# Kernel optimization log

Hardware: AMD Instinct MI355X
Metric: run time of the kernel (lower is better)

The kernel has to match this reference:

```python
import jax, jax.numpy as jnp
import numpy as np

B, N, NC = 16, 128, 32          # batch, num_vectors, num_condition_vectors
H, A, DEG = 256, 64, 3          # hidden_dim, attention_dim, degree
SCALE = float(np.sqrt(H) ** DEG)  # weights_scale = sqrt(hidden_dim)^degree = 4096
# S3 non-identity permutations lifted to batch tensor axes (batch axis 0 fixed)
PERMS = [(0, 1, 3, 2), (0, 2, 1, 3), (0, 2, 3, 1), (0, 3, 1, 2), (0, 3, 2, 1)]


def setup_inputs() -> dict:
    key = jax.random.key(0)
    ks = jax.random.split(key, 6)
    inv = 1.0 / np.sqrt(H)
    return {
        "x": jax.random.normal(ks[0], (B, N, H), jnp.float32),
        "x_mask": jnp.ones((B, N, 1), jnp.float32),
        "condition": jax.random.normal(ks[1], (B, NC, H), jnp.float32),
        "condition_mask": jnp.ones((B, NC, 1), jnp.float32),
        "W1": (jax.random.normal(ks[2], (DEG, H, H), jnp.float32) * inv),
        "b1": jnp.zeros((DEG, H), jnp.float32),
        "Wc": (jax.random.normal(ks[3], (DEG, H, H), jnp.float32) * inv),
        "Wlin": (jax.random.normal(ks[4], (DEG, H, A), jnp.float32) * inv),
        "blin": jnp.zeros((DEG, A), jnp.float32),
    }


def reference(x, x_mask, condition, condition_mask, W1, b1, Wc, Wlin, blin):
    # masked mean-pool of condition vectors: [B, H]
    pooled = (condition * condition_mask).sum(1) / jnp.maximum(condition_mask.sum(1), 1.0)
    ys, dvs = [], []
    for d in range(DEG):  # small fixed loop over structurally distinct branches
        dv = pooled @ Wc[d]                                   # daughter vector [B, H]
        h = jax.nn.gelu(x @ W1[d] + b1[d] + dv[:, None, :])   # branch encoder [B, N, H]
        y = (h @ Wlin[d] + blin[d]) * x_mask                  # linear + mask  [B, N, A]
        ys.append(y)
        dvs.append(dv)
    # degree-3 multilinear contraction: 'xbi,ybi,zbi->bxyz' == 'bxi,byi,bzi->bxyz'
    base = jnp.einsum('bxi,byi,bzi->bxyz', ys[0], ys[1], ys[2]) / SCALE
    # symmetrize: add all non-identity permuted views (S3 minus identity)
    out = base
    for p in PERMS:
        out = out + jnp.transpose(base, p)
    return out, jnp.stack(dvs)  # ([B,N,N,N], [DEG,B,H])
```

## Files before the change

### kernel.cpp

```cpp
#include <hip/hip_runtime.h>
#include <hip/hip_bf16.h>
#include <math.h>
#include <string.h>

#define BB   16
#define NN   128
#define NCC  32
#define HH   256
#define AA   64
#define DEGN 3
#define BNR  (BB*NN)

typedef __bf16 bf16x8 __attribute__((ext_vector_type(8)));
typedef float  f32x16 __attribute__((ext_vector_type(16)));

__device__ __forceinline__ unsigned int pk2(float lo, float hi) {
    __hip_bfloat162 h2 = __float22bfloat162_rn(make_float2(lo, hi));
    unsigned int u;
    memcpy(&u, &h2, 4);
    return u;
}
__device__ __forceinline__ float2 unpk(unsigned int u) {
    return make_float2(__uint_as_float(u << 16),
                       __uint_as_float(u & 0xffff0000u));
}
__device__ __forceinline__ unsigned short bfbits(float f) {
    __hip_bfloat16 h = __float2bfloat16(f);
    unsigned short u;
    memcpy(&u, &h, 2);
    return u;
}

__global__ __launch_bounds__(256) void k_head(const float* __restrict__ cond,
                                              const float* __restrict__ cmask,
                                              const float* __restrict__ Wc,
                                              const float* __restrict__ W1,
                                              const float* __restrict__ Wlin,
                                              float* __restrict__ dv,
                                              float* __restrict__ dv_out,
                                              unsigned short* __restrict__ W1t,
                                              unsigned short* __restrict__ Wlt) {
    __shared__ float shm[32 * 33];
    const int bid = blockIdx.x, t = threadIdx.x;

    if (bid < 48) {
        const int d = bid >> 4, b = bid & 15;
        float s = 0.f, ms = 0.f;
        for (int c = 0; c < NCC; ++c) {
            float mk = cmask[b * NCC + c];
            s  += cond[(b * NCC + c) * HH + t] * mk;
            ms += mk;
        }
        shm[t] = s / fmaxf(ms, 1.0f);
        __syncthreads();
        const float* Wd = Wc + (size_t)d * HH * HH;
        float acc = 0.f;
        for (int k = 0; k < HH; ++k) acc += shm[k] * Wd[k * HH + t];
        int idx = (d * BB + b) * HH + t;
        dv[idx]     = acc;
        dv_out[idx] = acc;
    } else if (bid < 240) {
        const int q = bid - 48;
        const int d = q >> 6, r2 = q & 63, tk = r2 >> 3, tn = r2 & 7;
        float (*tile)[33] = (float (*)[33])shm;
        #pragma unroll
        for (int p = 0; p < 4; ++p) {
            int kr = p * 8 + (t >> 5), nr = t & 31;
            tile[kr][nr] = W1[((size_t)d * HH + tk * 32 + kr) * HH + tn * 32 + nr];
        }
        __syncthreads();
        #pragma unroll
        for (int p = 0; p < 4; ++p) {
            int nr = p * 8 + (t >> 5), kr = t & 31;
            W1t[((size_t)d * HH + tn * 32 + nr) * HH + tk * 32 + kr] =
                bfbits(tile[kr][nr]);
        }
    } else {
        const int q = bid - 240;
        const int d = q >> 4, r3 = q & 15, tk = r3 >> 1, ta = r3 & 1;
        float (*tile)[33] = (float (*)[33])shm;
        #pragma unroll
        for (int p = 0; p < 4; ++p) {
            int kr = p * 8 + (t >> 5), ar = t & 31;
            tile[kr][ar] = Wlin[((size_t)d * HH + tk * 32 + kr) * AA + ta * 32 + ar];
        }
        __syncthreads();
        #pragma unroll
        for (int p = 0; p < 4; ++p) {
            int ar = p * 8 + (t >> 5), kr = t & 31;
            Wlt[((size_t)d * AA + ta * 32 + ar) * HH + tk * 32 + kr] =
                bfbits(tile[kr][ar]);
        }
    }
}

__global__ __launch_bounds__(256) void k_mlp(const float* __restrict__ x,
                                             const float* __restrict__ xmask,
                                             const float* __restrict__ b1,
                                             const float* __restrict__ blin,
                                             const float* __restrict__ dv,
                                             const unsigned short* __restrict__ W1t,
                                             const unsigned short* __restrict__ Wlt,
                                             float* __restrict__ yv) {
    __shared__ __align__(16) char ldsA[32 * 512];
    __shared__ float ps[2][32][68];

    const int t = threadIdx.x;
    const int d = blockIdx.x >> 6, rt = blockIdx.x & 63;
    const int row0 = rt * 32;
    const int b = row0 >> 7;
    const int lane = t & 63, wid = t >> 6;
    const int rl5 = lane & 31, h2v = lane >> 5;

    #pragma unroll
    for (int it = 0; it < 8; ++it) {
        const int r = wid * 8 + it;
        const float4 v = *(const float4*)&x[(size_t)(row0 + r) * HH + lane * 4];
        uint2 u = make_uint2(pk2(v.x, v.y), pk2(v.z, v.w));
        *(uint2*)(ldsA + r * 512 + ((lane * 8) ^ ((r & 7) << 4))) = u;
    }
    __syncthreads();

    f32x16 acc1[2];
    #pragma unroll
    for (int nt = 0; nt < 2; ++nt)
        #pragma unroll
        for (int e = 0; e < 16; ++e) acc1[nt][e] = 0.f;

    #pragma unroll
    for (int ks = 0; ks < 16; ++ks) {
        bf16x8 af = *(const bf16x8*)(ldsA + rl5 * 512 +
                      ((ks * 32 + h2v * 16) ^ ((rl5 & 7) << 4)));
        #pragma unroll
        for (int nt = 0; nt < 2; ++nt) {
            const int n = wid * 64 + nt * 32 + rl5;
            bf16x8 bf = *(const bf16x8*)(W1t +
                          ((size_t)d * HH + n) * HH + ks * 16 + h2v * 8);
            acc1[nt] = __builtin_amdgcn_mfma_f32_32x32x16_bf16(af, bf, acc1[nt], 0, 0, 0);
        }
    }
    __syncthreads();

    #pragma unroll
    for (int nt = 0; nt < 2; ++nt) {
        const int col = wid * 64 + nt * 32 + rl5;
        const float add = b1[d * HH + col] + dv[(d * BB + b) * HH + col];
        #pragma unroll
        for (int e = 0; e < 16; ++e) {
            const int row = (e & 3) + 8 * (e >> 2) + 4 * h2v;
            float v = acc1[nt][e] + add;
            float u = 0.7978845608028654f * (v + 0.044715f * v * v * v);
            float g = 0.5f * v * (1.0f + tanhf(u));
            *(unsigned short*)(ldsA + row * 512 + ((col * 2) ^ ((row & 7) << 4))) =
                bfbits(g);
        }
    }
    __syncthreads();

    const int qc = wid >> 1, kh = wid & 1;
    f32x16 acc2;
    #pragma unroll
    for (int e = 0; e < 16; ++e) acc2[e] = 0.f;
    #pragma unroll
    for (int ks = 0; ks < 8; ++ks) {
        const int kk = kh * 8 + ks;
        bf16x8 af = *(const bf16x8*)(ldsA + rl5 * 512 +
                      ((kk * 32 + h2v * 16) ^ ((rl5 & 7) << 4)));
        bf16x8 bf = *(const bf16x8*)(Wlt +
                      ((size_t)d * AA + qc * 32 + rl5) * HH + kk * 16 + h2v * 8);
        acc2 = __builtin_amdgcn_mfma_f32_32x32x16_bf16(af, bf, acc2, 0, 0, 0);
    }
    #pragma unroll
    for (int e = 0; e < 16; ++e) {
        const int row = (e & 3) + 8 * (e >> 2) + 4 * h2v;
        ps[kh][row][qc * 32 + rl5] = acc2[e];
    }
    __syncthreads();

    #pragma unroll
    for (int j = 0; j < 8; ++j) {
        const int idx = t * 8 + j;
        const int row = idx >> 6, a = idx & 63;
        float v = ps[0][row][a] + ps[1][row][a] + blin[d * AA + a];
        v *= xmask[row0 + row];
        yv[((size_t)d * BNR + row0 + row) * AA + a] = v;
    }
}

__device__ __forceinline__ void lds_fence_barrier() {
    asm volatile("s_waitcnt lgkmcnt(0)" ::: "memory");
    __builtin_amdgcn_s_barrier();
    __builtin_amdgcn_sched_barrier(0);
}
__device__ __forceinline__ void lds_wave_wait() {
    asm volatile("s_waitcnt lgkmcnt(0)" ::: "memory");
    __builtin_amdgcn_sched_barrier(0);
}

#define LROW 128

__global__ __launch_bounds__(512, 4) void k_contract(const float* __restrict__ yv,
                                                     float* __restrict__ outp) {
    __shared__ __align__(16) char lds[5 * 128 * LROW];
    char* A1b = lds;
    char* A2b = lds + 1 * 128 * LROW;
    char* Y0b = lds + 2 * 128 * LROW;
    char* B1b = lds + 3 * 128 * LROW;
    char* B2b = lds + 4 * 128 * LROW;

    const int t  = threadIdx.x;
    const int b  = blockIdx.x >> 5;
    const int xg = blockIdx.x & 31;

    const float* y0p = yv + (size_t)(0 * BNR + b * NN) * AA;
    const float* y1p = yv + (size_t)(1 * BNR + b * NN) * AA;
    const float* y2p = yv + (size_t)(2 * BNR + b * NN) * AA;

    const int lane = t & 63;
    const int wid  = t >> 6;
    const int li   = lane & 31;
    const int rh   = lane >> 5;
    const int rl5  = lane & 31, h2v = lane >> 5;
    const int wr   = wid >> 1, wc = wid & 1;

    float s0v[4], s1v[4], s2v[4];
    #pragma unroll
    for (int xi = 0; xi < 4; ++xi) {
        const int xr = xg * 4 + xi;
        s0v[xi] = y0p[xr * AA + lane];
        s1v[xi] = y1p[xr * AA + lane];
        s2v[xi] = y2p[xr * AA + lane];
    }

    #pragma unroll
    for (int it = 0; it < 8; ++it) {
        const int r   = wid * 16 + it * 2 + rh;
        const int swz = (r & 7) << 4;
        const int off = r * LROW + ((4 * li) ^ swz);
        const float2 v0 = *(const float2*)&y0p[r * AA + 2 * li];
        const float2 v1 = *(const float2*)&y1p[r * AA + 2 * li];
        const float2 v2 = *(const float2*)&y2p[r * AA + 2 * li];
        *(unsigned int*)(Y0b + off) = pk2(v0.x, v0.y);
        *(unsigned int*)(B1b + off) = pk2(v2.x, v2.y);
        *(unsigned int*)(B2b + off) = pk2(v1.x, v1.y);
    }

    const float inv = 1.0f / 4096.0f;
    float* scrf = (float*)(A1b + wid * 2048);

    #pragma unroll
    for (int xi = 0; xi < 4; ++xi) {
        const int xr = xg * 4 + xi;
        const float s0a = __shfl(s0v[xi], 2 * li), s0b = __shfl(s0v[xi], 2 * li + 1);
        const float s1a = __shfl(s1v[xi], 2 * li), s1b = __shfl(s1v[xi], 2 * li + 1);
        const float s2a = __shfl(s2v[xi], 2 * li), s2b = __shfl(s2v[xi], 2 * li + 1);

        if (xi == 0) lds_fence_barrier();

        #pragma unroll
        for (int it = 0; it < 8; ++it) {
            const int r   = wid * 16 + it * 2 + rh;
            const int swz = (r & 7) << 4;
            const int off = r * LROW + ((4 * li) ^ swz);
            const float2 y0 = unpk(*(const unsigned int*)(Y0b + off));
            const float2 y1 = unpk(*(const unsigned int*)(B2b + off));
            *(unsigned int*)(A1b + off) =
                pk2(s0a * y1.x + s1a * y0.x, s0b * y1.y + s1b * y0.y);
            *(unsigned int*)(A2b + off) = pk2(s2a * y0.x, s2b * y0.y);
        }
        lds_fence_barrier();

        f32x16 acc[2];
        #pragma unroll
        for (int ni = 0; ni < 2; ++ni)
            #pragma unroll
            for (int e = 0; e < 16; ++e) acc[ni][e] = 0.f;

        #pragma unroll
        for (int p = 0; p < 4; ++p) {
            const char* Ua = (p == 0) ? A1b : (p == 1) ? B1b : (p == 2) ? A2b : B2b;
            const char* Va = (p == 0) ? B1b : (p == 1) ? A1b : (p == 2) ? B2b : A2b;
            #pragma unroll
            for (int ks = 0; ks < 4; ++ks) {
                const int arow = wr * 32 + rl5;
                bf16x8 af = *(const bf16x8*)(Ua + arow * LROW +
                              ((ks * 32 + h2v * 16) ^ ((arow & 7) << 4)));
                #pragma unroll
                for (int ni = 0; ni < 2; ++ni) {
                    const int brow = wc * 64 + ni * 32 + rl5;
                    bf16x8 bf = *(const bf16x8*)(Va + brow * LROW +
                                  ((ks * 32 + h2v * 16) ^ ((brow & 7) << 4)));
                    acc[ni] = __builtin_amdgcn_mfma_f32_32x32x16_bf16(
                        af, bf, acc[ni], 0, 0, 0);
                }
            }
        }
        lds_fence_barrier();

        float* osl = outp + ((size_t)(b * NN + xr)) * (NN * NN);
        #pragma unroll
        for (int q = 0; q < 4; ++q) {
            #pragma unroll
            for (int ni = 0; ni < 2; ++ni) {
                #pragma unroll
                for (int j = 0; j < 4; ++j) {
                    const int e = q * 4 + j;
                    scrf[(j + 4 * h2v) * 64 + ni * 32 + rl5] = acc[ni][e] * inv;
                }
            }
            lds_wave_wait();
            #pragma unroll
            for (int r2 = 0; r2 < 8; ++r2) {
                float v = scrf[r2 * 64 + lane];
                osl[(size_t)(wr * 32 + q * 8 + r2) * NN + wc * 64 + lane] = v;
            }
            lds_wave_wait();
        }
    }
}

extern "C" void kernel_launch(void* const* d_in, const int* in_sizes, int n_in,
                              void* d_out, int out_size, void* d_ws, size_t ws_size,
                              hipStream_t stream) {
    const float* x     = (const float*)d_in[0];
    const float* xmask = (const float*)d_in[1];
    const float* cond  = (const float*)d_in[2];
    const float* cmask = (const float*)d_in[3];
    const float* W1    = (const float*)d_in[4];
    const float* b1    = (const float*)d_in[5];
    const float* Wc    = (const float*)d_in[6];
    const float* Wlin  = (const float*)d_in[7];
    const float* blin  = (const float*)d_in[8];

    float* out = (float*)d_out;
    float* ws  = (float*)d_ws;

    float* dv  = ws;
    float* yv  = ws + 12288;
    unsigned short* W1t = (unsigned short*)((char*)d_ws + (size_t)(12288 + 393216) * 4);
    unsigned short* Wlt = W1t + (size_t)DEGN * HH * HH;
    float* dv_out = out + (size_t)BB * NN * NN * NN;

    k_head    <<<dim3(288), dim3(256), 0, stream>>>(cond, cmask, Wc, W1, Wlin,
                                                    dv, dv_out, W1t, Wlt);
    k_mlp     <<<dim3(DEGN * 64), dim3(256), 0, stream>>>(x, xmask, b1, blin, dv,
                                                          W1t, Wlt, yv);
    k_contract<<<dim3(BB * NN / 4), dim3(512), 0, stream>>>(yv, out);
}
```

Before: 58.88 us.

## Overlap output stores with next slice MFMAs and drop LDS staging

The contraction kernel now double-buffers its accumulators, so the global stores for slice xi-1 are interleaved with the MFMA loop of slice xi instead of running after it. B rows are remapped to interleave the two 32-column tiles (brow = 2*rl5+ni), which lets each lane write adjacent float2 pairs directly to global memory and removes the LDS scratch transpose. The swizzle is changed to depend on r>>1 to match the new row access pattern. This costs extra accumulator registers and relies on float2 stores being coalesced well enough.

```diff
diff --git a/kernel.cpp b/kernel.cpp
--- a/kernel.cpp
+++ b/kernel.cpp
@@ -192,12 +192,9 @@
     __builtin_amdgcn_s_barrier();
     __builtin_amdgcn_sched_barrier(0);
 }
-__device__ __forceinline__ void lds_wave_wait() {
-    asm volatile("s_waitcnt lgkmcnt(0)" ::: "memory");
-    __builtin_amdgcn_sched_barrier(0);
-}
 
 #define LROW 128
+#define SWZ(r) ((((r) >> 1) & 7) << 4)
 
 __global__ __launch_bounds__(512, 4) void k_contract(const float* __restrict__ yv,
                                                      float* __restrict__ outp) {
@@ -222,6 +219,7 @@
     const int rh   = lane >> 5;
     const int rl5  = lane & 31, h2v = lane >> 5;
     const int wr   = wid >> 1, wc = wid & 1;
+    const float inv = 1.0f / 4096.0f;
 
     float s0v[4], s1v[4], s2v[4];
     #pragma unroll
@@ -235,8 +233,7 @@
     #pragma unroll
     for (int it = 0; it < 8; ++it) {
         const int r   = wid * 16 + it * 2 + rh;
-        const int swz = (r & 7) << 4;
-        const int off = r * LROW + ((4 * li) ^ swz);
+        const int off = r * LROW + ((4 * li) ^ SWZ(r));
         const float2 v0 = *(const float2*)&y0p[r * AA + 2 * li];
         const float2 v1 = *(const float2*)&y1p[r * AA + 2 * li];
         const float2 v2 = *(const float2*)&y2p[r * AA + 2 * li];
@@ -245,23 +242,18 @@
         *(unsigned int*)(B2b + off) = pk2(v1.x, v1.y);
     }
 
-    const float inv = 1.0f / 4096.0f;
-    float* scrf = (float*)(A1b + wid * 2048);
-
-    #pragma unroll
-    for (int xi = 0; xi < 4; ++xi) {
-        const int xr = xg * 4 + xi;
+    f32x16 accA[2], accB[2];
+
+    auto xi_step = [&](int xi, f32x16 (&cur)[2], f32x16 (&prv)[2],
+                       float* oslPrev, bool doStore) {
         const float s0a = __shfl(s0v[xi], 2 * li), s0b = __shfl(s0v[xi], 2 * li + 1);
         const float s1a = __shfl(s1v[xi], 2 * li), s1b = __shfl(s1v[xi], 2 * li + 1);
         const float s2a = __shfl(s2v[xi], 2 * li), s2b = __shfl(s2v[xi], 2 * li + 1);
 
-        if (xi == 0) lds_fence_barrier();
-
         #pragma unroll
         for (int it = 0; it < 8; ++it) {
             const int r   = wid * 16 + it * 2 + rh;
-            const int swz = (r & 7) << 4;
-            const int off = r * LROW + ((4 * li) ^ swz);
+            const int off = r * LROW + ((4 * li) ^ SWZ(r));
             const float2 y0 = unpk(*(const unsigned int*)(Y0b + off));
             const float2 y1 = unpk(*(const unsigned int*)(B2b + off));
             *(unsigned int*)(A1b + off) =
@@ -270,11 +262,10 @@
         }
         lds_fence_barrier();
 
-        f32x16 acc[2];
         #pragma unroll
         for (int ni = 0; ni < 2; ++ni)
             #pragma unroll
-            for (int e = 0; e < 16; ++e) acc[ni][e] = 0.f;
+            for (int e = 0; e < 16; ++e) cur[ni][e] = 0.f;
 
         #pragma unroll
         for (int p = 0; p < 4; ++p) {
@@ -284,38 +275,44 @@
             for (int ks = 0; ks < 4; ++ks) {
                 const int arow = wr * 32 + rl5;
                 bf16x8 af = *(const bf16x8*)(Ua + arow * LROW +
-                              ((ks * 32 + h2v * 16) ^ ((arow & 7) << 4)));
+                              ((ks * 32 + h2v * 16) ^ SWZ(arow)));
                 #pragma unroll
                 for (int ni = 0; ni < 2; ++ni) {
-                    const int brow = wc * 64 + ni * 32 + rl5;
+                    const int brow = wc * 64 + 2 * rl5 + ni;
                     bf16x8 bf = *(const bf16x8*)(Va + brow * LROW +
-                                  ((ks * 32 + h2v * 16) ^ ((brow & 7) << 4)));
-                    acc[ni] = __builtin_amdgcn_mfma_f32_32x32x16_bf16(
-                        af, bf, acc[ni], 0, 0, 0);
+                                  ((ks * 32 + h2v * 16) ^ SWZ(brow)));
+                    cur[ni] = __builtin_amdgcn_mfma_f32_32x32x16_bf16(
+                        af, bf, cur[ni], 0, 0, 0);
                 }
             }
-        }
-        lds_fence_barrier();
-
-        float* osl = outp + ((size_t)(b * NN + xr)) * (NN * NN);
-        #pragma unroll
-        for (int q = 0; q < 4; ++q) {
-            #pragma unroll
-            for (int ni = 0; ni < 2; ++ni) {
+            if (doStore) {
                 #pragma unroll
                 for (int j = 0; j < 4; ++j) {
-                    const int e = q * 4 + j;
-                    scrf[(j + 4 * h2v) * 64 + ni * 32 + rl5] = acc[ni][e] * inv;
+                    const int e    = p * 4 + j;
+                    const int rowf = wr * 32 + (e & 3) + 8 * (e >> 2) + 4 * h2v;
+                    float2 v = make_float2(prv[0][e] * inv, prv[1][e] * inv);
+                    *(float2*)&oslPrev[(size_t)rowf * NN + wc * 64 + 2 * rl5] = v;
                 }
+                __builtin_amdgcn_sched_barrier(0);
             }
-            lds_wave_wait();
-            #pragma unroll
-            for (int r2 = 0; r2 < 8; ++r2) {
-                float v = scrf[r2 * 64 + lane];
-                osl[(size_t)(wr * 32 + q * 8 + r2) * NN + wc * 64 + lane] = v;
-            }
-            lds_wave_wait();
-        }
+        }
+        lds_fence_barrier();
+    };
+
+    float* oslBase = outp + ((size_t)(b * NN + xg * 4)) * (NN * NN);
+
+    lds_fence_barrier();
+    xi_step(0, accA, accB, nullptr,               false);
+    xi_step(1, accB, accA, oslBase + 0 * NN * NN, true);
+    xi_step(2, accA, accB, oslBase + 1 * NN * NN, true);
+    xi_step(3, accB, accA, oslBase + 2 * NN * NN, true);
+
+    float* osl3 = oslBase + 3 * NN * NN;
+    #pragma unroll
+    for (int e = 0; e < 16; ++e) {
+        const int rowf = wr * 32 + (e & 3) + 8 * (e >> 2) + 4 * h2v;
+        float2 v = make_float2(accB[0][e] * inv, accB[1][e] * inv);
+        *(float2*)&osl3[(size_t)rowf * NN + wc * 64 + 2 * rl5] = v;
     }
 }
 
```

After: 63.94 us. 8.6% more time.
